# Optimization experiments

Hardware: AMD Instinct MI355X
Metric: run time of the kernel (lower is better)

The kernel has to match this reference:

```python
import jax, jax.numpy as jnp
import numpy as np

N_NODE = 20000
N_EDGE = 200000
EMBED = 256
PAIR = 128
HEADS = 16
HEAD_DIM = EMBED // HEADS
SCALING = HEAD_DIM ** -0.5
EPS = 1e-5


def _ln(x, w, b):
    m = x.mean(-1, keepdims=True)
    v = ((x - m) ** 2).mean(-1, keepdims=True)
    return (x - m) / jnp.sqrt(v + EPS) * w + b


def setup_inputs() -> dict:
    key = jax.random.key(0)
    ks = jax.random.split(key, 12)
    inp = {
        "query": jax.random.normal(ks[0], (N_NODE, EMBED), jnp.float32),
        "edge_index": jax.random.randint(ks[1], (N_EDGE, 2), 0, N_NODE, jnp.int64 if jax.config.jax_enable_x64 else jnp.int32),
        "edge_diff": jax.random.normal(ks[2], (N_EDGE, 3), jnp.float32),
        "pair": jax.random.normal(ks[3], (N_EDGE, PAIR), jnp.float32),
        "ln_w": jnp.ones((EMBED,), jnp.float32),
        "ln_b": jnp.zeros((EMBED,), jnp.float32),
        "pln_w": jnp.ones((PAIR,), jnp.float32),
        "pln_b": jnp.zeros((PAIR,), jnp.float32),
        "Wq": jax.random.normal(ks[4], (EMBED, EMBED), jnp.float32) * 0.02,
        "Wk": jax.random.normal(ks[5], (EMBED, EMBED), jnp.float32) * 0.02,
        "Wv": jax.random.normal(ks[6], (EMBED, EMBED), jnp.float32) * 0.02,
        "Wb": jax.random.normal(ks[7], (HEADS, PAIR), jnp.float32) * 0.02,
        "bb": jnp.zeros((HEADS,), jnp.float32),
        "Wf1": jax.random.normal(ks[8], (1, EMBED), jnp.float32) * 0.02,
        "bf1": jnp.zeros((1,), jnp.float32),
        "Wf2": jax.random.normal(ks[9], (1, EMBED), jnp.float32) * 0.02,
        "bf2": jnp.zeros((1,), jnp.float32),
        "Wf3": jax.random.normal(ks[10], (1, EMBED), jnp.float32) * 0.02,
        "bf3": jnp.zeros((1,), jnp.float32),
    }
    return inp


def reference(query, edge_index, edge_diff, pair, ln_w, ln_b, pln_w, pln_b,
              Wq, Wk, Wv, Wb, bb, Wf1, bf1, Wf2, bf2, Wf3, bf3):
    n_node = query.shape[0]
    src = edge_index[:, 0]
    dst = edge_index[:, 1]

    qn = _ln(query, ln_w, ln_b)          # preln on node features
    pn = _ln(pair, pln_w, pln_b)         # preln on pair features

    q = (qn @ Wq.T).reshape(n_node, HEADS, HEAD_DIM)
    k = (qn @ Wk.T).reshape(n_node, HEADS, HEAD_DIM)
    v = (qn @ Wv.T).reshape(n_node, HEADS, HEAD_DIM)

    qe = q[src] * SCALING                # [E,H,D]
    ke = k[dst]
    ve = v[dst]

    logits = (qe * ke).sum(-1) + pn @ Wb.T + bb   # [E,H]

    # segment softmax over destination node (edge_index[:,0])
    seg_max = jax.ops.segment_max(logits, src, num_segments=n_node)  # [N,H]
    ex = jnp.exp(logits - seg_max[src])
    denom = jax.ops.segment_sum(ex, src, num_segments=n_node)
    probs = ex / denom[src]              # [E,H]

    # 3D-weighted scatter-sum: out[n,h,c,d] = sum_e probs[e,h]*diff[e,c]*v[e,h,d]
    w = probs[:, :, None] * edge_diff[:, None, :]                    # [E,H,3]
    contrib = w[:, :, :, None] * ve[:, :, None, :]                   # [E,H,3,D]
    x = jax.ops.segment_sum(contrib, src, num_segments=n_node)       # [N,H,3,D]
    x = x.transpose(0, 2, 1, 3).reshape(n_node, 3, EMBED)            # [N,3,H*D]

    f1 = x[:, 0, :] @ Wf1.T + bf1
    f2 = x[:, 1, :] @ Wf2.T + bf2
    f3 = x[:, 2, :] @ Wf3.T + bf3
    return jnp.concatenate([f1, f2, f3], axis=-1).astype(jnp.float32)
```

## Files before the change

kernel.cpp:

```cpp
#include <hip/hip_runtime.h>
#include <math.h>

#define N_NODE 20000
#define N_EDGE 200000
#define EMBED 256
#define PAIR 128
#define HEADS 16
#define HEAD_DIM 16
#define SCALING 0.25f
#define LNEPS 1e-5f

typedef unsigned short u16;
typedef unsigned int u32;
typedef __attribute__((ext_vector_type(8))) short bf16x8;
typedef __attribute__((ext_vector_type(4))) float f32x4;

#define WS_QKV   0
#define WS_QN    30720000
#define WS_WBF   40960000
#define WS_WW    41353216
#define WS_C0    41357312
#define WS_C1    41357376
#define WS_BIAS  41357440
#define WS_VW    54157440
#define WS_CNT   57997440
#define WS_CUR   58077440
#define WS_OFF   58157440
#define WS_DE    58237504

__device__ __forceinline__ u16 f2bf(float f) {
  u32 u = __float_as_uint(f);
  u32 r = (u + 0x7FFFu + ((u >> 16) & 1u)) >> 16;
  return (u16)r;
}
__device__ __forceinline__ float bl(u32 u) { return __uint_as_float(u << 16); }
__device__ __forceinline__ float bh(u32 u) { return __uint_as_float(u & 0xFFFF0000u); }

__device__ __forceinline__ float dot8(uint4 a, uint4 b) {
  float s = bl(a.x) * bl(b.x) + bh(a.x) * bh(b.x);
  s += bl(a.y) * bl(b.y) + bh(a.y) * bh(b.y);
  s += bl(a.z) * bl(b.z) + bh(a.z) * bh(b.z);
  s += bl(a.w) * bl(b.w) + bh(a.w) * bh(b.w);
  return s;
}

__global__ __launch_bounds__(256) void k1_pre_kernel(
    const float* __restrict__ query, const float* __restrict__ ln_w,
    const float* __restrict__ ln_b, u16* __restrict__ qn,
    int* __restrict__ counts, int* __restrict__ cur,
    const float* __restrict__ Wq, const float* __restrict__ Wk,
    const float* __restrict__ Wv, u16* __restrict__ Wbf,
    const float* __restrict__ pln_w, const float* __restrict__ pln_b,
    const float* __restrict__ Wb, const float* __restrict__ bb,
    u16* __restrict__ WWbf, float* __restrict__ c0, float* __restrict__ c1) {
  int bid = blockIdx.x;
  if (bid < 5000) {
    int z = bid * 256 + threadIdx.x;
    if (z < N_NODE) { counts[z] = 0; cur[z] = 0; }
    int node = bid * 4 + (threadIdx.x >> 6);
    int lane = threadIdx.x & 63;
    float4 a = *(const float4*)(query + (size_t)node * EMBED + lane * 4);
    float s = a.x + a.y + a.z + a.w;
    float s2 = a.x * a.x + a.y * a.y + a.z * a.z + a.w * a.w;
    #pragma unroll
    for (int off = 32; off > 0; off >>= 1) {
      s += __shfl_xor(s, off);
      s2 += __shfl_xor(s2, off);
    }
    float m = s * (1.0f / EMBED);
    float r = rsqrtf(s2 * (1.0f / EMBED) - m * m + LNEPS);
    float4 w4 = *(const float4*)(ln_w + lane * 4);
    float4 b4 = *(const float4*)(ln_b + lane * 4);
    ushort4 st;
    st.x = f2bf((a.x - m) * r * w4.x + b4.x);
    st.y = f2bf((a.y - m) * r * w4.y + b4.y);
    st.z = f2bf((a.z - m) * r * w4.z + b4.z);
    st.w = f2bf((a.w - m) * r * w4.w + b4.w);
    *(ushort4*)(qn + (size_t)node * EMBED + lane * 4) = st;
  } else if (bid < 5192) {
    int g4 = (bid - 5000) * 256 + threadIdx.x;
    int idx = g4 * 4;
    const float* src = (idx < 65536) ? Wq : (idx < 131072 ? Wk : Wv);
    float4 v = *(const float4*)(src + (idx & 65535));
    ushort4 st = {f2bf(v.x), f2bf(v.y), f2bf(v.z), f2bf(v.w)};
    *(ushort4*)(Wbf + idx) = st;
  } else if (threadIdx.x < 64) {
    int l = threadIdx.x;
    for (int h = 0; h < HEADS; h++) {
      int i0 = l * 2;
      float wb0 = Wb[h * PAIR + i0], wb1 = Wb[h * PAIR + i0 + 1];
      float ww0 = pln_w[i0] * wb0, ww1 = pln_w[i0 + 1] * wb1;
      WWbf[h * PAIR + i0] = f2bf(ww0);
      WWbf[h * PAIR + i0 + 1] = f2bf(ww1);
      float s1 = ww0 + ww1;
      float s0 = pln_b[i0] * wb0 + pln_b[i0 + 1] * wb1;
      #pragma unroll
      for (int off = 32; off > 0; off >>= 1) {
        s1 += __shfl_xor(s1, off);
        s0 += __shfl_xor(s0, off);
      }
      if (l == 0) {
        c1[h] = s1;
        c0[h] = s0 + bb[h];
      }
    }
  }
}

#define BKP 72
__global__ __launch_bounds__(256, 2) void k2_gemm_hist_kernel(
    const u16* __restrict__ qn, const u16* __restrict__ Wbf,
    u16* __restrict__ qkv, const int* __restrict__ edge_index,
    int* __restrict__ counts) {
  __shared__ u16 As[128 * BKP];
  __shared__ u16 Bs[128 * BKP];
  int bid = blockIdx.x;
  if (bid >= 942) {
    int e = (bid - 942) * 256 + threadIdx.x;
    if (e < N_EDGE) atomicAdd(&counts[edge_index[e * 2]], 1);
    return;
  }
  int bx = bid % 157, by = bid / 157;
  int t = threadIdx.x;
  int wv = t >> 6, lane = t & 63;
  int quad = lane >> 4, l16 = lane & 15;
  int row0 = bx * 128, col0 = by * 128;
  int mt = (wv >> 1) * 64, nt = (wv & 1) * 64;

  f32x4 acc[4][4];
  #pragma unroll
  for (int im = 0; im < 4; im++)
    #pragma unroll
    for (int in_ = 0; in_ < 4; in_++) acc[im][in_] = (f32x4){0.f, 0.f, 0.f, 0.f};

  for (int it = 0; it < 4; it++) {
    int k0 = it * 64;
    #pragma unroll
    for (int j = 0; j < 4; j++) {
      int L = j * 256 + t;
      int row = L >> 3, slot = L & 7;
      int ra = min(row0 + row, N_NODE - 1);
      uint4 va = *(const uint4*)(qn + (size_t)ra * 256 + k0 + slot * 8);
      *(uint4*)(&As[row * BKP + slot * 8]) = va;
      uint4 vb = *(const uint4*)(Wbf + (size_t)(col0 + row) * 256 + k0 + slot * 8);
      *(uint4*)(&Bs[row * BKP + slot * 8]) = vb;
    }
    __syncthreads();
    #pragma unroll
    for (int s = 0; s < 2; s++) {
      int ko = s * 32 + quad * 8;
      bf16x8 af[4], bf[4];
      #pragma unroll
      for (int im = 0; im < 4; im++)
        af[im] = *(const bf16x8*)(&As[(mt + im * 16 + l16) * BKP + ko]);
      #pragma unroll
      for (int in_ = 0; in_ < 4; in_++)
        bf[in_] = *(const bf16x8*)(&Bs[(nt + in_ * 16 + l16) * BKP + ko]);
      #pragma unroll
      for (int im = 0; im < 4; im++)
        #pragma unroll
        for (int in_ = 0; in_ < 4; in_++)
          acc[im][in_] = __builtin_amdgcn_mfma_f32_16x16x32_bf16(
              af[im], bf[in_], acc[im][in_], 0, 0, 0);
    }
    __syncthreads();
  }
  #pragma unroll
  for (int im = 0; im < 4; im++) {
    #pragma unroll
    for (int in_ = 0; in_ < 4; in_++) {
      int gcol = col0 + nt + in_ * 16 + l16;
      float scale = (gcol < 256) ? SCALING : 1.0f;
      #pragma unroll
      for (int r = 0; r < 4; r++) {
        int grow = row0 + mt + im * 16 + quad * 4 + r;
        if (grow < N_NODE)
          qkv[(size_t)grow * 768 + gcol] = f2bf(acc[im][in_][r] * scale);
      }
    }
  }
}

__global__ __launch_bounds__(1024) void scan_kernel(
    const int* __restrict__ counts, int* __restrict__ off) {
  __shared__ int part[1024];
  int t = threadIdx.x;
  int loc[20];
  int s = 0;
  #pragma unroll
  for (int i = 0; i < 20; i++) {
    int idx = t * 20 + i;
    int v = (idx < N_NODE) ? counts[idx] : 0;
    loc[i] = s;
    s += v;
  }
  part[t] = s;
  __syncthreads();
  int x = s;
  for (int o = 1; o < 1024; o <<= 1) {
    int y = (t >= o) ? part[t - o] : 0;
    __syncthreads();
    x += y;
    part[t] = x;
    __syncthreads();
  }
  int excl = x - s;
  #pragma unroll
  for (int i = 0; i < 20; i++) {
    int idx = t * 20 + i;
    if (idx < N_NODE) off[idx] = excl + loc[i];
  }
  if (t == 0) off[N_NODE] = N_EDGE;
}

#define PP 136
__global__ __launch_bounds__(256) void k4_bias_vw_scatter_kernel(
    const float* __restrict__ pair, const u16* __restrict__ WWbf,
    const float* __restrict__ c0g, const float* __restrict__ c1g,
    float* __restrict__ bias, const u16* __restrict__ qkv,
    const float* __restrict__ Wf1, const float* __restrict__ Wf2,
    const float* __restrict__ Wf3, float* __restrict__ vw,
    const int* __restrict__ edge_index, const int* __restrict__ off,
    int* __restrict__ cur, int2* __restrict__ de) {
  __shared__ u16 Ps[64 * PP];
  __shared__ u16 WWs[16 * PP];
  __shared__ float ms[64], rs[64], c0s[16], c1s[16];
  int bid = blockIdx.x;
  int t = threadIdx.x;
  if (bid >= 4375) {
    int e = (bid - 4375) * 256 + t;
    if (e < N_EDGE) {
      int src = edge_index[e * 2 + 0];
      int dst = edge_index[e * 2 + 1];
      int pos = off[src] + atomicAdd(&cur[src], 1);
      de[pos] = make_int2(dst, e);
    }
    return;
  }
  if (bid >= 3125) {
    int gid = (bid - 3125) * 256 + t;
    int n = gid >> 4, h = gid & 15;
    const uint4* vp = (const uint4*)(qkv + (size_t)n * 768 + 512 + h * 16);
    uint4 va = vp[0], vb = vp[1];
    float v[16];
    v[0] = bl(va.x); v[1] = bh(va.x); v[2] = bl(va.y); v[3] = bh(va.y);
    v[4] = bl(va.z); v[5] = bh(va.z); v[6] = bl(va.w); v[7] = bh(va.w);
    v[8] = bl(vb.x); v[9] = bh(vb.x); v[10] = bl(vb.y); v[11] = bh(vb.y);
    v[12] = bl(vb.z); v[13] = bh(vb.z); v[14] = bl(vb.w); v[15] = bh(vb.w);
    const float* wf[3] = {Wf1 + h * 16, Wf2 + h * 16, Wf3 + h * 16};
    #pragma unroll
    for (int c = 0; c < 3; c++) {
      float s = 0.f;
      #pragma unroll
      for (int d = 0; d < 16; d++) s += v[d] * wf[c][d];
      vw[(size_t)n * 48 + h * 3 + c] = s;
    }
    return;
  }
  int wv = t >> 6, lane = t & 63;
  int quad = lane >> 4, l16 = lane & 15;
  int e0 = bid * 64;
  #pragma unroll
  for (int j = 0; j < 8; j++) {
    int L = j * 256 + t;
    int row = L >> 5, slot = L & 31;
    float4 p = *(const float4*)(pair + (size_t)(e0 + row) * PAIR + slot * 4);
    ushort4 st = {f2bf(p.x), f2bf(p.y), f2bf(p.z), f2bf(p.w)};
    *(ushort4*)(&Ps[row * PP + slot * 4]) = st;
  }
  #pragma unroll
  for (int j = 0; j < 2; j++) {
    int L = j * 256 + t;
    int row = L >> 5, slot = L & 31;
    ushort4 w = *(const ushort4*)(WWbf + row * PAIR + slot * 4);
    *(ushort4*)(&WWs[row * PP + slot * 4]) = w;
  }
  if (t < 16) {
    c0s[t] = c0g[t];
    c1s[t] = c1g[t];
  }
  __syncthreads();
  {
    int row = t >> 2, qq = t & 3;
    float s = 0.f, s2 = 0.f;
    #pragma unroll
    for (int jj = 0; jj < 8; jj++) {
      ushort4 u = *(const ushort4*)(&Ps[row * PP + (qq * 8 + jj) * 4]);
      float x0 = __uint_as_float((u32)u.x << 16);
      float x1 = __uint_as_float((u32)u.y << 16);
      float x2 = __uint_as_float((u32)u.z << 16);
      float x3 = __uint_as_float((u32)u.w << 16);
      s += x0 + x1 + x2 + x3;
      s2 += x0 * x0 + x1 * x1 + x2 * x2 + x3 * x3;
    }
    s += __shfl_xor(s, 1); s += __shfl_xor(s, 2);
    s2 += __shfl_xor(s2, 1); s2 += __shfl_xor(s2, 2);
    if (qq == 0) {
      float m = s * (1.0f / PAIR);
      ms[row] = m;
      rs[row] = rsqrtf(s2 * (1.0f / PAIR) - m * m + LNEPS);
    }
  }
  __syncthreads();
  f32x4 acc = (f32x4){0.f, 0.f, 0.f, 0.f};
  #pragma unroll
  for (int sk = 0; sk < 4; sk++) {
    int ko = sk * 32 + quad * 8;
    bf16x8 a = *(const bf16x8*)(&Ps[(wv * 16 + l16) * PP + ko]);
    bf16x8 b = *(const bf16x8*)(&WWs[l16 * PP + ko]);
    acc = __builtin_amdgcn_mfma_f32_16x16x32_bf16(a, b, acc, 0, 0, 0);
  }
  #pragma unroll
  for (int r = 0; r < 4; r++) {
    int el = wv * 16 + quad * 4 + r;
    float bv = rs[el] * (acc[r] - ms[el] * c1s[l16]) + c0s[l16];
    bias[(size_t)(e0 + el) * HEADS + l16] = bv;
  }
}

__global__ __launch_bounds__(256) void seg_attn_kernel(
    const u16* __restrict__ qkv, const float* __restrict__ bias,
    const int* __restrict__ off, const int2* __restrict__ de,
    const float* __restrict__ vw, const float* __restrict__ edge_diff,
    const float* __restrict__ bf1, const float* __restrict__ bf2,
    const float* __restrict__ bf3, float* __restrict__ out) {
  int wv = threadIdx.x >> 6, lane = threadIdx.x & 63;
  int src = blockIdx.x * 4 + wv;
  int h = lane & 15, eslot = lane >> 4;
  int lo = off[src];
  int deg = off[src + 1] - lo;
  const uint4* qp = (const uint4*)(qkv + (size_t)src * 768 + h * 16);
  uint4 q0 = qp[0], q1 = qp[1];
  float exsum = 0.f, a0 = 0.f, a1 = 0.f, a2 = 0.f;
  for (int ei = eslot; ei < deg; ei += 4) {
    int2 d_e = de[lo + ei];
    const uint4* kp = (const uint4*)(qkv + (size_t)d_e.x * 768 + 256 + h * 16);
    float d = dot8(q0, kp[0]) + dot8(q1, kp[1]);
    float ex = __expf(d + bias[(size_t)d_e.y * HEADS + h]);
    exsum += ex;
    const float* vp = vw + (size_t)d_e.x * 48 + h * 3;
    const float* dp = edge_diff + (size_t)d_e.y * 3;
    a0 += ex * vp[0] * dp[0];
    a1 += ex * vp[1] * dp[1];
    a2 += ex * vp[2] * dp[2];
  }
  exsum += __shfl_xor(exsum, 16);
  exsum += __shfl_xor(exsum, 32);
  float rden = (exsum > 0.f) ? 1.0f / exsum : 0.f;
  a0 *= rden; a1 *= rden; a2 *= rden;
  #pragma unroll
  for (int o = 1; o < 64; o <<= 1) {
    a0 += __shfl_xor(a0, o);
    a1 += __shfl_xor(a1, o);
    a2 += __shfl_xor(a2, o);
  }
  if (lane == 0) {
    out[src * 3 + 0] = a0 + bf1[0];
    out[src * 3 + 1] = a1 + bf2[0];
    out[src * 3 + 2] = a2 + bf3[0];
  }
}

extern "C" void kernel_launch(void* const* d_in, const int* in_sizes, int n_in,
                              void* d_out, int out_size, void* d_ws,
                              size_t ws_size, hipStream_t stream) {
  const float* query      = (const float*)d_in[0];
  const int*   edge_index = (const int*)d_in[1];
  const float* edge_diff  = (const float*)d_in[2];
  const float* pair       = (const float*)d_in[3];
  const float* ln_w       = (const float*)d_in[4];
  const float* ln_b       = (const float*)d_in[5];
  const float* pln_w      = (const float*)d_in[6];
  const float* pln_b      = (const float*)d_in[7];
  const float* Wq         = (const float*)d_in[8];
  const float* Wk         = (const float*)d_in[9];
  const float* Wv         = (const float*)d_in[10];
  const float* Wb         = (const float*)d_in[11];
  const float* bb         = (const float*)d_in[12];
  const float* Wf1        = (const float*)d_in[13];
  const float* bf1        = (const float*)d_in[14];
  const float* Wf2        = (const float*)d_in[15];
  const float* bf2        = (const float*)d_in[16];
  const float* Wf3        = (const float*)d_in[17];
  const float* bf3        = (const float*)d_in[18];

  char* ws = (char*)d_ws;
  u16*   qkv   = (u16*)(ws + WS_QKV);
  u16*   qn    = (u16*)(ws + WS_QN);
  u16*   Wbf   = (u16*)(ws + WS_WBF);
  u16*   WWbf  = (u16*)(ws + WS_WW);
  float* c0    = (float*)(ws + WS_C0);
  float* c1    = (float*)(ws + WS_C1);
  float* bias  = (float*)(ws + WS_BIAS);
  float* vw    = (float*)(ws + WS_VW);
  int*   counts= (int*)(ws + WS_CNT);
  int*   cur   = (int*)(ws + WS_CUR);
  int*   off   = (int*)(ws + WS_OFF);
  int2*  de    = (int2*)(ws + WS_DE);
  float* out   = (float*)d_out;

  k1_pre_kernel<<<5193, 256, 0, stream>>>(query, ln_w, ln_b, qn, counts, cur,
                                          Wq, Wk, Wv, Wbf, pln_w, pln_b, Wb,
                                          bb, WWbf, c0, c1);
  k2_gemm_hist_kernel<<<1724, 256, 0, stream>>>(qn, Wbf, qkv, edge_index,
                                                counts);
  scan_kernel<<<1, 1024, 0, stream>>>(counts, off);
  k4_bias_vw_scatter_kernel<<<5157, 256, 0, stream>>>(
      pair, WWbf, c0, c1, bias, qkv, Wf1, Wf2, Wf3, vw, edge_index, off, cur,
      de);
  seg_attn_kernel<<<N_NODE / 4, 256, 0, stream>>>(qkv, bias, off, de, vw,
                                                  edge_diff, bf1, bf2, bf3,
                                                  out);
}
```

Measured before the change: 292.1 us.

## Fuse histogram, scan and scatter into neighbouring kernels; store bias in CSR order

The edge-count histogram moves into the preprocessing kernel, and the scan becomes an extra block of the GEMM kernel, which removes the standalone single-block scan launch. The edge scatter is folded into the bias kernel. It writes 16-byte records holding dst and edge_diff at the CSR position, and it writes bias rows at that sorted position, so the attention kernel reads bias and diff contiguously instead of gathering them by edge id. The counters are zeroed with a memset. The trade-offs are that the scan runs serially within each thread over 79 elements, and that bias writes become scattered.

```diff
diff --git a/kernel.cpp b/kernel.cpp
--- a/kernel.cpp
+++ b/kernel.cpp
@@ -26,7 +26,7 @@
 #define WS_CNT   57997440
 #define WS_CUR   58077440
 #define WS_OFF   58157440
-#define WS_DE    58237504
+#define WS_REC   58237504
 
 __device__ __forceinline__ u16 f2bf(float f) {
   u32 u = __float_as_uint(f);
@@ -44,19 +44,17 @@
   return s;
 }
 
-__global__ __launch_bounds__(256) void k1_pre_kernel(
+__global__ __launch_bounds__(256) void k1_pre_hist_kernel(
     const float* __restrict__ query, const float* __restrict__ ln_w,
     const float* __restrict__ ln_b, u16* __restrict__ qn,
-    int* __restrict__ counts, int* __restrict__ cur,
     const float* __restrict__ Wq, const float* __restrict__ Wk,
     const float* __restrict__ Wv, u16* __restrict__ Wbf,
     const float* __restrict__ pln_w, const float* __restrict__ pln_b,
     const float* __restrict__ Wb, const float* __restrict__ bb,
-    u16* __restrict__ WWbf, float* __restrict__ c0, float* __restrict__ c1) {
+    u16* __restrict__ WWbf, float* __restrict__ c0, float* __restrict__ c1,
+    const int* __restrict__ edge_index, int* __restrict__ counts) {
   int bid = blockIdx.x;
   if (bid < 5000) {
-    int z = bid * 256 + threadIdx.x;
-    if (z < N_NODE) { counts[z] = 0; cur[z] = 0; }
     int node = bid * 4 + (threadIdx.x >> 6);
     int lane = threadIdx.x & 63;
     float4 a = *(const float4*)(query + (size_t)node * EMBED + lane * 4);
@@ -84,44 +82,68 @@
     float4 v = *(const float4*)(src + (idx & 65535));
     ushort4 st = {f2bf(v.x), f2bf(v.y), f2bf(v.z), f2bf(v.w)};
     *(ushort4*)(Wbf + idx) = st;
-  } else if (threadIdx.x < 64) {
-    int l = threadIdx.x;
-    for (int h = 0; h < HEADS; h++) {
-      int i0 = l * 2;
-      float wb0 = Wb[h * PAIR + i0], wb1 = Wb[h * PAIR + i0 + 1];
-      float ww0 = pln_w[i0] * wb0, ww1 = pln_w[i0 + 1] * wb1;
-      WWbf[h * PAIR + i0] = f2bf(ww0);
-      WWbf[h * PAIR + i0 + 1] = f2bf(ww1);
-      float s1 = ww0 + ww1;
-      float s0 = pln_b[i0] * wb0 + pln_b[i0 + 1] * wb1;
-      #pragma unroll
-      for (int off = 32; off > 0; off >>= 1) {
-        s1 += __shfl_xor(s1, off);
-        s0 += __shfl_xor(s0, off);
+  } else if (bid == 5192) {
+    if (threadIdx.x < 64) {
+      int l = threadIdx.x;
+      for (int h = 0; h < HEADS; h++) {
+        int i0 = l * 2;
+        float wb0 = Wb[h * PAIR + i0], wb1 = Wb[h * PAIR + i0 + 1];
+        float ww0 = pln_w[i0] * wb0, ww1 = pln_w[i0 + 1] * wb1;
+        WWbf[h * PAIR + i0] = f2bf(ww0);
+        WWbf[h * PAIR + i0 + 1] = f2bf(ww1);
+        float s1 = ww0 + ww1;
+        float s0 = pln_b[i0] * wb0 + pln_b[i0 + 1] * wb1;
+        #pragma unroll
+        for (int off = 32; off > 0; off >>= 1) {
+          s1 += __shfl_xor(s1, off);
+          s0 += __shfl_xor(s0, off);
+        }
+        if (l == 0) {
+          c1[h] = s1;
+          c0[h] = s0 + bb[h];
+        }
       }
-      if (l == 0) {
-        c1[h] = s1;
-        c0[h] = s0 + bb[h];
-      }
-    }
+    }
+  } else {
+    int e = (bid - 5193) * 256 + threadIdx.x;
+    if (e < N_EDGE) atomicAdd(&counts[edge_index[e * 2]], 1);
   }
 }
 
 #define BKP 72
-__global__ __launch_bounds__(256, 2) void k2_gemm_hist_kernel(
+__global__ __launch_bounds__(256, 2) void k2_gemm_scan_kernel(
     const u16* __restrict__ qn, const u16* __restrict__ Wbf,
-    u16* __restrict__ qkv, const int* __restrict__ edge_index,
-    int* __restrict__ counts) {
+    u16* __restrict__ qkv, const int* __restrict__ counts,
+    int* __restrict__ off) {
+  int bid = blockIdx.x;
+  int t = threadIdx.x;
+  if (bid == 942) {
+    __shared__ int part[256];
+    int i0 = t * 79;
+    int i1 = i0 + 79; if (i1 > N_NODE) i1 = N_NODE;
+    int s = 0;
+    for (int i = i0; i < i1; i++) s += counts[i];
+    part[t] = s;
+    __syncthreads();
+    int x = s;
+    for (int o = 1; o < 256; o <<= 1) {
+      int y = (t >= o) ? part[t - o] : 0;
+      __syncthreads();
+      x += y;
+      part[t] = x;
+      __syncthreads();
+    }
+    int run = x - s;
+    for (int i = i0; i < i1; i++) {
+      off[i] = run;
+      run += counts[i];
+    }
+    if (t == 255) off[N_NODE] = N_EDGE;
+    return;
+  }
   __shared__ u16 As[128 * BKP];
   __shared__ u16 Bs[128 * BKP];
-  int bid = blockIdx.x;
-  if (bid >= 942) {
-    int e = (bid - 942) * 256 + threadIdx.x;
-    if (e < N_EDGE) atomicAdd(&counts[edge_index[e * 2]], 1);
-    return;
-  }
   int bx = bid % 157, by = bid / 157;
-  int t = threadIdx.x;
   int wv = t >> 6, lane = t & 63;
   int quad = lane >> 4, l16 = lane & 15;
   int row0 = bx * 128, col0 = by * 128;
@@ -181,62 +203,18 @@
   }
 }
 
-__global__ __launch_bounds__(1024) void scan_kernel(
-    const int* __restrict__ counts, int* __restrict__ off) {
-  __shared__ int part[1024];
-  int t = threadIdx.x;
-  int loc[20];
-  int s = 0;
-  #pragma unroll
-  for (int i = 0; i < 20; i++) {
-    int idx = t * 20 + i;
-    int v = (idx < N_NODE) ? counts[idx] : 0;
-    loc[i] = s;
-    s += v;
-  }
-  part[t] = s;
-  __syncthreads();
-  int x = s;
-  for (int o = 1; o < 1024; o <<= 1) {
-    int y = (t >= o) ? part[t - o] : 0;
-    __syncthreads();
-    x += y;
-    part[t] = x;
-    __syncthreads();
-  }
-  int excl = x - s;
-  #pragma unroll
-  for (int i = 0; i < 20; i++) {
-    int idx = t * 20 + i;
-    if (idx < N_NODE) off[idx] = excl + loc[i];
-  }
-  if (t == 0) off[N_NODE] = N_EDGE;
-}
-
 #define PP 136
-__global__ __launch_bounds__(256) void k4_bias_vw_scatter_kernel(
+__global__ __launch_bounds__(256) void k3_bias_scatter_vw_kernel(
     const float* __restrict__ pair, const u16* __restrict__ WWbf,
     const float* __restrict__ c0g, const float* __restrict__ c1g,
     float* __restrict__ bias, const u16* __restrict__ qkv,
     const float* __restrict__ Wf1, const float* __restrict__ Wf2,
     const float* __restrict__ Wf3, float* __restrict__ vw,
-    const int* __restrict__ edge_index, const int* __restrict__ off,
-    int* __restrict__ cur, int2* __restrict__ de) {
-  __shared__ u16 Ps[64 * PP];
-  __shared__ u16 WWs[16 * PP];
-  __shared__ float ms[64], rs[64], c0s[16], c1s[16];
+    const int* __restrict__ edge_index, const float* __restrict__ edge_diff,
+    const int* __restrict__ off, int* __restrict__ cur,
+    uint4* __restrict__ rec) {
   int bid = blockIdx.x;
   int t = threadIdx.x;
-  if (bid >= 4375) {
-    int e = (bid - 4375) * 256 + t;
-    if (e < N_EDGE) {
-      int src = edge_index[e * 2 + 0];
-      int dst = edge_index[e * 2 + 1];
-      int pos = off[src] + atomicAdd(&cur[src], 1);
-      de[pos] = make_int2(dst, e);
-    }
-    return;
-  }
   if (bid >= 3125) {
     int gid = (bid - 3125) * 256 + t;
     int n = gid >> 4, h = gid & 15;
@@ -257,6 +235,10 @@
     }
     return;
   }
+  __shared__ u16 Ps[64 * PP];
+  __shared__ u16 WWs[16 * PP];
+  __shared__ float ms[64], rs[64], c0s[16], c1s[16];
+  __shared__ int pos_s[64];
   int wv = t >> 6, lane = t & 63;
   int quad = lane >> 4, l16 = lane & 15;
   int e0 = bid * 64;
@@ -278,6 +260,20 @@
   if (t < 16) {
     c0s[t] = c0g[t];
     c1s[t] = c1g[t];
+  }
+  if (t < 64) {
+    int e = e0 + t;
+    int srcn = edge_index[e * 2 + 0];
+    int dstn = edge_index[e * 2 + 1];
+    int pos = off[srcn] + atomicAdd(&cur[srcn], 1);
+    pos_s[t] = pos;
+    const float* dp = edge_diff + (size_t)e * 3;
+    uint4 r;
+    r.x = (u32)dstn;
+    r.y = __float_as_uint(dp[0]);
+    r.z = __float_as_uint(dp[1]);
+    r.w = __float_as_uint(dp[2]);
+    rec[pos] = r;
   }
   __syncthreads();
   {
@@ -314,16 +310,16 @@
   for (int r = 0; r < 4; r++) {
     int el = wv * 16 + quad * 4 + r;
     float bv = rs[el] * (acc[r] - ms[el] * c1s[l16]) + c0s[l16];
-    bias[(size_t)(e0 + el) * HEADS + l16] = bv;
+    bias[(size_t)pos_s[el] * HEADS + l16] = bv;
   }
 }
 
 __global__ __launch_bounds__(256) void seg_attn_kernel(
     const u16* __restrict__ qkv, const float* __restrict__ bias,
-    const int* __restrict__ off, const int2* __restrict__ de,
-    const float* __restrict__ vw, const float* __restrict__ edge_diff,
-    const float* __restrict__ bf1, const float* __restrict__ bf2,
-    const float* __restrict__ bf3, float* __restrict__ out) {
+    const int* __restrict__ off, const uint4* __restrict__ rec,
+    const float* __restrict__ vw, const float* __restrict__ bf1,
+    const float* __restrict__ bf2, const float* __restrict__ bf3,
+    float* __restrict__ out) {
   int wv = threadIdx.x >> 6, lane = threadIdx.x & 63;
   int src = blockIdx.x * 4 + wv;
   int h = lane & 15, eslot = lane >> 4;
@@ -333,16 +329,19 @@
   uint4 q0 = qp[0], q1 = qp[1];
   float exsum = 0.f, a0 = 0.f, a1 = 0.f, a2 = 0.f;
   for (int ei = eslot; ei < deg; ei += 4) {
-    int2 d_e = de[lo + ei];
-    const uint4* kp = (const uint4*)(qkv + (size_t)d_e.x * 768 + 256 + h * 16);
+    uint4 rr = rec[lo + ei];
+    int dst = (int)rr.x;
+    float d0 = __uint_as_float(rr.y);
+    float d1 = __uint_as_float(rr.z);
+    float d2 = __uint_as_float(rr.w);
+    const uint4* kp = (const uint4*)(qkv + (size_t)dst * 768 + 256 + h * 16);
     float d = dot8(q0, kp[0]) + dot8(q1, kp[1]);
-    float ex = __expf(d + bias[(size_t)d_e.y * HEADS + h]);
+    float ex = __expf(d + bias[(size_t)(lo + ei) * HEADS + h]);
     exsum += ex;
-    const float* vp = vw + (size_t)d_e.x * 48 + h * 3;
-    const float* dp = edge_diff + (size_t)d_e.y * 3;
-    a0 += ex * vp[0] * dp[0];
-    a1 += ex * vp[1] * dp[1];
-    a2 += ex * vp[2] * dp[2];
+    const float* vp = vw + (size_t)dst * 48 + h * 3;
+    a0 += ex * vp[0] * d0;
+    a1 += ex * vp[1] * d1;
+    a2 += ex * vp[2] * d2;
   }
   exsum += __shfl_xor(exsum, 16);
   exsum += __shfl_xor(exsum, 32);
@@ -396,19 +395,17 @@
   int*   counts= (int*)(ws + WS_CNT);
   int*   cur   = (int*)(ws + WS_CUR);
   int*   off   = (int*)(ws + WS_OFF);
-  int2*  de    = (int2*)(ws + WS_DE);
+  uint4* rec   = (uint4*)(ws + WS_REC);
   float* out   = (float*)d_out;
 
-  k1_pre_kernel<<<5193, 256, 0, stream>>>(query, ln_w, ln_b, qn, counts, cur,
-                                          Wq, Wk, Wv, Wbf, pln_w, pln_b, Wb,
-                                          bb, WWbf, c0, c1);
-  k2_gemm_hist_kernel<<<1724, 256, 0, stream>>>(qn, Wbf, qkv, edge_index,
-                                                counts);
-  scan_kernel<<<1, 1024, 0, stream>>>(counts, off);
-  k4_bias_vw_scatter_kernel<<<5157, 256, 0, stream>>>(
-      pair, WWbf, c0, c1, bias, qkv, Wf1, Wf2, Wf3, vw, edge_index, off, cur,
-      de);
-  seg_attn_kernel<<<N_NODE / 4, 256, 0, stream>>>(qkv, bias, off, de, vw,
-                                                  edge_diff, bf1, bf2, bf3,
-                                                  out);
-}
+  hipMemsetAsync(ws + WS_CNT, 0, 160000, stream);
+  k1_pre_hist_kernel<<<5975, 256, 0, stream>>>(
+      query, ln_w, ln_b, qn, Wq, Wk, Wv, Wbf, pln_w, pln_b, Wb, bb, WWbf, c0,
+      c1, edge_index, counts);
+  k2_gemm_scan_kernel<<<943, 256, 0, stream>>>(qn, Wbf, qkv, counts, off);
+  k3_bias_scatter_vw_kernel<<<4375, 256, 0, stream>>>(
+      pair, WWbf, c0, c1, bias, qkv, Wf1, Wf2, Wf3, vw, edge_index, edge_diff,
+      off, cur, rec);
+  seg_attn_kernel<<<N_NODE / 4, 256, 0, stream>>>(qkv, bias, off, rec, vw,
+                                                  bf1, bf2, bf3, out);
+}
```

Result: slower. 305.3 us (+4.5%).
